# Kernel optimization log

Hardware: AMD Instinct MI355X
Metric: run time of the kernel (lower is better)

The kernel has to match this reference:

```python
import jax, jax.numpy as jnp
import numpy as np

BN_EPS = 1e-5
INTERP_EPS = 1e-8


def setup_inputs() -> dict:
    key = jax.random.key(0)
    ks = jax.random.split(key, 8)
    B, N, S, D1, D2 = 8, 8192, 2048, 128, 256
    C_in, C_mid, C_out = D1 + D2, 256, 256
    return {
        "xyz1": jax.random.normal(ks[0], (B, 3, N), dtype=jnp.float32),
        "xyz2": jax.random.normal(ks[1], (B, 3, S), dtype=jnp.float32),
        "points1": jax.random.normal(ks[2], (B, D1, N), dtype=jnp.float32),
        "points2": jax.random.normal(ks[3], (B, D2, S), dtype=jnp.float32),
        "W0": jax.random.normal(ks[4], (C_mid, C_in), dtype=jnp.float32) * (1.0 / np.sqrt(C_in)),
        "b0": jnp.zeros((C_mid,), dtype=jnp.float32),
        "gamma0": jnp.ones((C_mid,), dtype=jnp.float32),
        "beta0": jnp.zeros((C_mid,), dtype=jnp.float32),
        "W1": jax.random.normal(ks[5], (C_out, C_mid), dtype=jnp.float32) * (1.0 / np.sqrt(C_mid)),
        "b1": jnp.zeros((C_out,), dtype=jnp.float32),
    }


def reference(xyz1, xyz2, points1, points2, W0, b0, gamma0, beta0, W1, b1):
    B, _, N = xyz1.shape
    S = xyz2.shape[2]
    x1 = jnp.transpose(xyz1, (0, 2, 1))  # (B, N, 3)
    x2 = jnpp = jnp.transpose(xyz2, (0, 2, 1))  # (B, S, 3)
    # squared distances: (B, N, S)
    d = (jnp.sum(x1 ** 2, -1)[:, :, None]
         + jnp.sum(x2 ** 2, -1)[:, None, :]
         - 2.0 * jnp.einsum('bnc,bsc->bns', x1, x2))
    # 3 nearest neighbors (fused top-3 instead of full sort; same math)
    neg_d, idx = jax.lax.top_k(-d, 3)  # (B, N, 3)
    dists = -neg_d
    recip = 1.0 / (dists + INTERP_EPS)
    weight = recip / jnp.sum(recip, axis=2, keepdims=True)  # (B, N, 3)
    p2t = jnp.transpose(points2, (0, 2, 1))  # (B, S, D2)
    D2 = p2t.shape[-1]
    gathered = jnp.take_along_axis(p2t, idx.reshape(B, N * 3, 1), axis=1).reshape(B, N, 3, D2)
    interp = jnp.einsum('bnkc,bnk->bcn', gathered, weight)  # (B, D2, N)
    new_points = jnp.concatenate([interp, points1], axis=1)  # (B, D2+D1, N)
    # conv0 (1x1) + BatchNorm (train mode, batch stats) + ReLU
    h = jnp.einsum('oc,bcn->bon', W0, new_points) + b0[None, :, None]
    mean = jnp.mean(h, axis=(0, 2), keepdims=True)
    var = jnp.mean((h - mean) ** 2, axis=(0, 2), keepdims=True)  # biased, as torch BN
    h = gamma0[None, :, None] * (h - mean) * jax.lax.rsqrt(var + BN_EPS) + beta0[None, :, None]
    h = jax.nn.relu(h)
    # conv1 (1x1) + Identity (module pairs conv1 with nn.Identity) + ReLU
    h = jnp.einsum('oc,bcn->bon', W1, h) + b1[None, :, None]
    return jax.nn.relu(h)
```

## Files before the change

kernel.cpp:

```cpp
#include <hip/hip_runtime.h>
#include <stdint.h>

constexpr int B = 8, N = 8192, S = 2048, D1 = 128, D2 = 256;
constexpr int CIN = 384, CMID = 256, COUT = 256;

typedef __attribute__((ext_vector_type(8))) _Float16 half8;
typedef __attribute__((ext_vector_type(4))) _Float16 half4;
typedef __attribute__((ext_vector_type(4))) float f32x4;

union HU { uint32_t u; _Float16 h[2]; };


__global__ __launch_bounds__(256) void k_top3(const float* __restrict__ xyz1,
                                              const float* __restrict__ xyz2,
                                              uint32_t* __restrict__ pw3) {
  __shared__ float md[4][3][64];
  __shared__ int mi[4][3][64];
  const int tid = threadIdx.x;
  const int wv = tid >> 6, lane = tid & 63;
  const int b = blockIdx.y;
  const int n = blockIdx.x * 64 + lane;
  const float* x1 = xyz1 + (size_t)b * 3 * N;
  const float ax = x1[n], ay = x1[n + N], az = x1[n + 2 * N];
  const float* x2 = xyz2 + (size_t)b * 3 * S;

  float d0 = 1e30f, d1 = 1e30f, d2 = 1e30f;
  int i0 = 0, i1 = 0, i2 = 0;
  const int s0 = wv * (S / 4), s1 = s0 + (S / 4);
#pragma unroll 8
  for (int s = s0; s < s1; ++s) {
    float sx = x2[s], sy = x2[s + S], sz = x2[s + 2 * S];
    float dx = ax - sx, dy = ay - sy, dz = az - sz;
    float d = dx * dx + dy * dy + dz * dz;
    if (d < d2) {
      if (d < d1) {
        d2 = d1; i2 = i1;
        if (d < d0) { d1 = d0; i1 = i0; d0 = d; i0 = s; }
        else        { d1 = d;  i1 = s; }
      } else { d2 = d; i2 = s; }
    }
  }
  md[wv][0][lane] = d0; mi[wv][0][lane] = i0;
  md[wv][1][lane] = d1; mi[wv][1][lane] = i1;
  md[wv][2][lane] = d2; mi[wv][2][lane] = i2;
  __syncthreads();
  if (tid < 64) {
    float e0 = md[0][0][tid], e1 = md[0][1][tid], e2 = md[0][2][tid];
    int j0 = mi[0][0][tid], j1 = mi[0][1][tid], j2 = mi[0][2][tid];
#pragma unroll
    for (int w = 1; w < 4; ++w)
#pragma unroll
      for (int k = 0; k < 3; ++k) {
        float d = md[w][k][tid];
        int i = mi[w][k][tid];
        if (d < e2) {
          if (d < e1) {
            e2 = e1; j2 = j1;
            if (d < e0) { e1 = e0; j1 = j0; e0 = d; j0 = i; }
            else        { e1 = d;  j1 = i; }
          } else { e2 = d; j2 = i; }
        }
      }
    float r0 = 1.0f / (e0 + 1e-8f), r1 = 1.0f / (e1 + 1e-8f), r2 = 1.0f / (e2 + 1e-8f);
    float inv = 1.0f / (r0 + r1 + r2);
    auto pack = [](int i, float w) -> uint32_t {
      uint32_t q = (uint32_t)(w * 2097152.0f + 0.5f);
      if (q > 0x1FFFFFu) q = 0x1FFFFFu;
      return ((uint32_t)i << 21) | q;
    };
    size_t base = ((size_t)b * N + blockIdx.x * 64 + tid) * 3;
    pw3[base]     = pack(j0, r0 * inv);
    pw3[base + 1] = pack(j1, r1 * inv);
    pw3[base + 2] = pack(j2, r2 * inv);
  }
}

__global__ __launch_bounds__(256) void k_G(const float* __restrict__ points2,
                                           const float* __restrict__ W0,
                                           float* __restrict__ dout) {
  __shared__ half8 A_lds[4][256];
  __shared__ half8 B_lds[4][32];
  __shared__ float CT[32][258];
  const int tid = threadIdx.x;
  const int b = blockIdx.x >> 6;
  const int s0 = (blockIdx.x & 63) * 32;
  f32x4 acc[4][2] = {};
  const int wv = tid >> 6, lane = tid & 63;
  const int ln = lane & 15, quad = lane >> 4;
  const int bn = tid & 31, bkc = tid >> 5;
  const int ar = tid >> 3, ac4 = tid & 7;

  for (int kk = 0; kk < 256; kk += 32) {
    __syncthreads();
#pragma unroll
    for (int p = 0; p < 8; ++p) {
      int row = ar + 32 * p;
      const float4 v = *(const float4*)(W0 + (size_t)row * CIN + kk + ac4 * 4);
      half4 hv = {(_Float16)v.x, (_Float16)v.y, (_Float16)v.z, (_Float16)v.w};
      *(half4*)((_Float16*)&A_lds[ac4 >> 1][row] + (ac4 & 1) * 4) = hv;
    }
    {
      half4 hv;
#pragma unroll
      for (int j = 0; j < 4; ++j)
        hv[j] = (_Float16)points2[((size_t)(b * 256 + kk + bkc * 4 + j)) * S + s0 + bn];
      *(half4*)((_Float16*)&B_lds[bkc >> 1][bn] + (bkc & 1) * 4) = hv;
    }
    __syncthreads();
    half8 af[4], bf[2];
#pragma unroll
    for (int i = 0; i < 4; ++i) af[i] = A_lds[quad][wv * 64 + i * 16 + ln];
#pragma unroll
    for (int j = 0; j < 2; ++j) bf[j] = B_lds[quad][j * 16 + ln];
#pragma unroll
    for (int i = 0; i < 4; ++i)
#pragma unroll
      for (int j = 0; j < 2; ++j)
        acc[i][j] = __builtin_amdgcn_mfma_f32_16x16x32_f16(af[i], bf[j], acc[i][j], 0, 0, 0);
  }
  __syncthreads();
#pragma unroll
  for (int i = 0; i < 4; ++i)
#pragma unroll
    for (int reg = 0; reg < 4; ++reg) {
      int row = wv * 64 + i * 16 + quad * 4 + reg;
#pragma unroll
      for (int j = 0; j < 2; ++j) CT[j * 16 + ln][row] = acc[i][j][reg];
    }
  __syncthreads();
  const int sl = tid >> 3, g = tid & 7;
  float* g0 = dout + ((size_t)(b * 256 + 128)) * 8192 + (size_t)(s0 + sl) * 256 + g * 32;
#pragma unroll
  for (int q = 0; q < 8; ++q)
    *(float4*)(g0 + q * 4) = *(const float4*)&CT[sl][g * 32 + q * 4];
}

__global__ __launch_bounds__(256) void k_interp(const uint32_t* __restrict__ pw3,
                                                const float* __restrict__ dout_c,
                                                uint32_t* __restrict__ dout_u) {
  __shared__ int sidx[96];
  __shared__ float sw[96];
  const int tid = threadIdx.x;
  const int b = blockIdx.x >> 8;
  const int n0 = (blockIdx.x & 255) * 32;
  if (tid < 96) {
    uint32_t p = pw3[((size_t)b * N + n0) * 3 + tid];
    sidx[tid] = (int)(p >> 21);
    sw[tid] = (float)(p & 0x1FFFFFu) * (1.0f / 2097152.0f);
  }
  __syncthreads();
  const int colL = tid >> 3, p = tid & 7;
  const float* Gb = dout_c + ((size_t)(b * 256 + 128)) * 8192;
  float a[32];
#pragma unroll
  for (int q = 0; q < 32; ++q) a[q] = 0.f;
#pragma unroll
  for (int k = 0; k < 3; ++k) {
    int j = sidx[colL * 3 + k];
    float w = sw[colL * 3 + k];
    const float* g = Gb + (size_t)j * 256 + p * 32;
#pragma unroll
    for (int q = 0; q < 8; ++q) {
      float4 v = *(const float4*)(g + q * 4);
      a[q * 4 + 0] += w * v.x; a[q * 4 + 1] += w * v.y;
      a[q * 4 + 2] += w * v.z; a[q * 4 + 3] += w * v.w;
    }
  }
#pragma unroll
  for (int q = 0; q < 16; ++q) {
    int cp = p * 16 + q;
    HU u;
    u.h[0] = (_Float16)a[2 * q];
    u.h[1] = (_Float16)a[2 * q + 1];
    dout_u[((size_t)(b * 256 + cp)) * 8192 + n0 + colL] = u.u;
  }
}

__global__ __launch_bounds__(256) void k_h(uint32_t* __restrict__ h2,
                                           float* __restrict__ dpart,
                                           const float* __restrict__ points1,
                                           const float* __restrict__ W0,
                                           const float* __restrict__ b0) {
  __shared__ half8 A_lds[4][256];
  __shared__ half8 B_lds[4][64];
  __shared__ float red_s[256], red_q[256], sb0[256];
  const int tid = threadIdx.x;
  const int b = blockIdx.x >> 7;
  const int cb = blockIdx.x & 127;
  const int n0 = cb * 64;
  sb0[tid] = b0[tid];
  f32x4 acc[4][4] = {};
  const int wv = tid >> 6, lane = tid & 63;
  const int ln = lane & 15, quad = lane >> 4;
  const int bn = tid & 63, bkc = tid >> 6;
  const int ar = tid >> 3, ac4 = tid & 7;

  for (int kk = 0; kk < 128; kk += 32) {
    __syncthreads();
#pragma unroll
    for (int p = 0; p < 8; ++p) {
      int row = ar + 32 * p;
      const float4 v = *(const float4*)(W0 + (size_t)row * CIN + 256 + kk + ac4 * 4);
      half4 hv = {(_Float16)v.x, (_Float16)v.y, (_Float16)v.z, (_Float16)v.w};
      *(half4*)((_Float16*)&A_lds[ac4 >> 1][row] + (ac4 & 1) * 4) = hv;
    }
    {
      half8 hv;
#pragma unroll
      for (int j = 0; j < 8; ++j)
        hv[j] = (_Float16)points1[((size_t)(b * D1 + kk + bkc * 8 + j)) * N + n0 + bn];
      B_lds[bkc][bn] = hv;
    }
    __syncthreads();
    half8 af[4], bf[4];
#pragma unroll
    for (int i = 0; i < 4; ++i) af[i] = A_lds[quad][wv * 64 + i * 16 + ln];
#pragma unroll
    for (int j = 0; j < 4; ++j) bf[j] = B_lds[quad][j * 16 + ln];
#pragma unroll
    for (int i = 0; i < 4; ++i)
#pragma unroll
      for (int j = 0; j < 4; ++j)
        acc[i][j] = __builtin_amdgcn_mfma_f32_16x16x32_f16(af[i], bf[j], acc[i][j], 0, 0, 0);
  }
#pragma unroll
  for (int i = 0; i < 4; ++i) {
    const int rb = wv * 64 + i * 16 + quad * 4;
    const int cp0 = rb >> 1;
    float rs[4] = {0.f, 0.f, 0.f, 0.f}, rq[4] = {0.f, 0.f, 0.f, 0.f};
#pragma unroll
    for (int jj = 0; jj < 4; ++jj) {
      const int col = n0 + jj * 16 + ln;
      size_t a0 = ((size_t)(b * 256 + cp0)) * 8192 + col;
      HU ua, ub;
      ua.u = h2[a0];
      ub.u = h2[a0 + 8192];
      _Float16 e0 = (_Float16)(acc[i][jj][0] + (float)ua.h[0] + sb0[rb + 0]);
      _Float16 e1 = (_Float16)(acc[i][jj][1] + (float)ua.h[1] + sb0[rb + 1]);
      _Float16 e2 = (_Float16)(acc[i][jj][2] + (float)ub.h[0] + sb0[rb + 2]);
      _Float16 e3 = (_Float16)(acc[i][jj][3] + (float)ub.h[1] + sb0[rb + 3]);
      HU o0, o1;
      o0.h[0] = e0; o0.h[1] = e1; o1.h[0] = e2; o1.h[1] = e3;
      h2[a0] = o0.u;
      h2[a0 + 8192] = o1.u;
      float f0 = (float)e0, f1 = (float)e1, f2 = (float)e2, f3 = (float)e3;
      rs[0] += f0; rq[0] += f0 * f0;
      rs[1] += f1; rq[1] += f1 * f1;
      rs[2] += f2; rq[2] += f2 * f2;
      rs[3] += f3; rq[3] += f3 * f3;
    }
#pragma unroll
    for (int reg = 0; reg < 4; ++reg) {
      float s = rs[reg], q = rq[reg];
#pragma unroll
      for (int m = 1; m < 16; m <<= 1) {
        s += __shfl_xor(s, m);
        q += __shfl_xor(q, m);
      }
      if (ln == 0) { red_s[rb + reg] = s; red_q[rb + reg] = q; }
    }
  }
  __syncthreads();
  float* part = dpart + ((size_t)(b * 256 + 192)) * 8192 + (size_t)cb * 512;
  part[tid] = red_s[tid];
  part[256 + tid] = red_q[tid];
}

__global__ __launch_bounds__(256) void k_bn(const float* __restrict__ dpart,
                                            const float* __restrict__ gamma,
                                            const float* __restrict__ beta,
                                            float* __restrict__ bna,
                                            float* __restrict__ bnb) {
  const int c = blockIdx.x;
  const int tid = threadIdx.x;
  float s = 0.f, q = 0.f;
#pragma unroll
  for (int u = tid; u < 1024; u += 256) {
    int b = u >> 7, cb = u & 127;
    const float* part = dpart + ((size_t)(b * 256 + 192)) * 8192 + (size_t)cb * 512;
    s += part[c];
    q += part[256 + c];
  }
#pragma unroll
  for (int m = 1; m < 64; m <<= 1) {
    s += __shfl_xor(s, m);
    q += __shfl_xor(q, m);
  }
  __shared__ float ls[4], lq[4];
  if ((tid & 63) == 0) { ls[tid >> 6] = s; lq[tid >> 6] = q; }
  __syncthreads();
  if (tid == 0) {
    float st = ls[0] + ls[1] + ls[2] + ls[3];
    float qt = lq[0] + lq[1] + lq[2] + lq[3];
    const float invn = 1.0f / (float)(B * N);
    float mean = st * invn;
    float var = qt * invn - mean * mean;
    float a = gamma[c] * rsqrtf(var + 1e-5f);
    bna[c] = a;
    bnb[c] = beta[c] - mean * a;
  }
}

__global__ __launch_bounds__(256) void k_fused1(const uint32_t* h2,
                                                const float* __restrict__ W1,
                                                const float* __restrict__ b1,
                                                const float* __restrict__ bna,
                                                const float* __restrict__ bnb,
                                                float* out) {
  __shared__ uint32_t Hh[32 * 65 * 4];
  __shared__ float sa[256], sb[256], sb1[256];
  const int tid = threadIdx.x;
  const int b = blockIdx.x >> 7;
  const int n0 = (blockIdx.x & 127) * 64;
  sa[tid] = bna[tid]; sb[tid] = bnb[tid]; sb1[tid] = b1[tid];
  __syncthreads();
  {
    const int col = tid & 63, cpb = tid >> 6;
#pragma unroll
    for (int q = 0; q < 32; ++q) {
      int cp = cpb * 32 + q;
      HU u;
      u.u = h2[((size_t)(b * 256 + cp)) * 8192 + n0 + col];
      int k0 = 2 * cp;
      float v0 = sa[k0] * (float)u.h[0] + sb[k0];
      float v1 = sa[k0 + 1] * (float)u.h[1] + sb[k0 + 1];
      HU o;
      o.h[0] = (_Float16)(v0 > 0.f ? v0 : 0.f);
      o.h[1] = (_Float16)(v1 > 0.f ? v1 : 0.f);
      Hh[((cp >> 2) * 65 + col) * 4 + (cp & 3)] = o.u;
    }
  }
  __syncthreads();
  f32x4 acc[4][4] = {};
  const int wv = tid >> 6, lane = tid & 63;
  const int ln = lane & 15, quad = lane >> 4;
  for (int kk = 0; kk < 256; kk += 32) {
    half8 af[4], bf[4];
#pragma unroll
    for (int i = 0; i < 4; ++i) {
      int row = wv * 64 + i * 16 + ln;
      const float* wr = W1 + (size_t)row * CMID + kk + quad * 8;
      float4 w0 = *(const float4*)wr;
      float4 w1v = *(const float4*)(wr + 4);
      af[i] = half8{(_Float16)w0.x, (_Float16)w0.y, (_Float16)w0.z, (_Float16)w0.w,
                    (_Float16)w1v.x, (_Float16)w1v.y, (_Float16)w1v.z, (_Float16)w1v.w};
    }
#pragma unroll
    for (int j = 0; j < 4; ++j)
      bf[j] = *(const half8*)&Hh[(((kk >> 3) + quad) * 65 + j * 16 + ln) * 4];
#pragma unroll
    for (int i = 0; i < 4; ++i)
#pragma unroll
      for (int j = 0; j < 4; ++j)
        acc[i][j] = __builtin_amdgcn_mfma_f32_16x16x32_f16(af[i], bf[j], acc[i][j], 0, 0, 0);
  }
#pragma unroll
  for (int i = 0; i < 4; ++i) {
    const int rb = wv * 64 + i * 16 + quad * 4;
#pragma unroll
    for (int reg = 0; reg < 4; ++reg) {
      int row = rb + reg;
      float bias = sb1[row];
      float* orow = out + ((size_t)(b * 256 + row)) * 8192 + n0;
#pragma unroll
      for (int j = 0; j < 4; ++j)
        orow[j * 16 + ln] = fmaxf(acc[i][j][reg] + bias, 0.f);
    }
  }
}

extern "C" void kernel_launch(void* const* d_in, const int* in_sizes, int n_in,
                              void* d_out, int out_size, void* d_ws, size_t ws_size,
                              hipStream_t stream) {
  const float* xyz1 = (const float*)d_in[0];
  const float* xyz2 = (const float*)d_in[1];
  const float* points1 = (const float*)d_in[2];
  const float* points2 = (const float*)d_in[3];
  const float* W0 = (const float*)d_in[4];
  const float* b0 = (const float*)d_in[5];
  const float* gamma0 = (const float*)d_in[6];
  const float* beta0 = (const float*)d_in[7];
  const float* W1 = (const float*)d_in[8];
  const float* b1 = (const float*)d_in[9];
  float* out = (float*)d_out;

  char* ws = (char*)d_ws;
  float* bna = (float*)ws;
  float* bnb = (float*)(ws + 1024);
  uint32_t* pw3 = (uint32_t*)(ws + 2048);

  k_top3<<<dim3(N / 64, B), 256, 0, stream>>>(xyz1, xyz2, pw3);
  k_G<<<dim3(B * 64), 256, 0, stream>>>(points2, W0, out);
  k_interp<<<dim3(B * N / 32), 256, 0, stream>>>(pw3, out, (uint32_t*)out);
  k_h<<<dim3(B * N / 64), 256, 0, stream>>>((uint32_t*)out, out, points1, W0, b0);
  k_bn<<<dim3(256), 256, 0, stream>>>(out, gamma0, beta0, bna, bnb);
  k_fused1<<<dim3(B * N / 64), 256, 0, stream>>>((const uint32_t*)out, W1, b1,
                                                 bna, bnb, out);
}
```

Measured before the change: 375.3 us.

## Stage xyz2 with norms in LDS and use branchless expanded-distance top-3

The top-3 search kernel now loads each batch's query points into shared memory as float4 (x, y, z, |s|^2) once per block. The inner loop computes a partial distance with three FMAs using the expanded form, adding the query norm only at the end. The branchy insertion sort is replaced by branchless selects plus med3/min updates. This cuts global loads, ALU work and divergence in the hot loop, at the cost of 32KB of LDS per block, which may lower occupancy, and slight numerical differences in the distances.

```diff
diff --git a/kernel.cpp b/kernel.cpp
--- a/kernel.cpp
+++ b/kernel.cpp
@@ -14,8 +14,10 @@
 __global__ __launch_bounds__(256) void k_top3(const float* __restrict__ xyz1,
                                               const float* __restrict__ xyz2,
                                               uint32_t* __restrict__ pw3) {
+  __shared__ float4 Pq[S];
   __shared__ float md[4][3][64];
   __shared__ int mi[4][3][64];
+  __shared__ float snrm[64];
   const int tid = threadIdx.x;
   const int wv = tid >> 6, lane = tid & 63;
   const int b = blockIdx.y;
@@ -24,44 +26,57 @@
   const float ax = x1[n], ay = x1[n + N], az = x1[n + 2 * N];
   const float* x2 = xyz2 + (size_t)b * 3 * S;
 
-  float d0 = 1e30f, d1 = 1e30f, d2 = 1e30f;
-  int i0 = 0, i1 = 0, i2 = 0;
+  for (int j = tid; j < S; j += 256) {
+    float sx = x2[j], sy = x2[j + S], sz = x2[j + 2 * S];
+    Pq[j] = float4{sx, sy, sz, sx * sx + sy * sy + sz * sz};
+  }
+  if (wv == 0) snrm[lane] = ax * ax + ay * ay + az * az;
+  __syncthreads();
+
+  const float nax = -2.f * ax, nay = -2.f * ay, naz = -2.f * az;
+  float e0 = 1e30f, e1 = 1e30f, e2 = 1e30f;
+  int j0 = 0, j1 = 0, j2 = 0;
   const int s0 = wv * (S / 4), s1 = s0 + (S / 4);
 #pragma unroll 8
   for (int s = s0; s < s1; ++s) {
-    float sx = x2[s], sy = x2[s + S], sz = x2[s + 2 * S];
-    float dx = ax - sx, dy = ay - sy, dz = az - sz;
-    float d = dx * dx + dy * dy + dz * dz;
-    if (d < d2) {
-      if (d < d1) {
-        d2 = d1; i2 = i1;
-        if (d < d0) { d1 = d0; i1 = i0; d0 = d; i0 = s; }
-        else        { d1 = d;  i1 = s; }
-      } else { d2 = d; i2 = s; }
-    }
-  }
-  md[wv][0][lane] = d0; mi[wv][0][lane] = i0;
-  md[wv][1][lane] = d1; mi[wv][1][lane] = i1;
-  md[wv][2][lane] = d2; mi[wv][2][lane] = i2;
+    const float4 v = Pq[s];
+    const float d = fmaf(nax, v.x, fmaf(nay, v.y, fmaf(naz, v.z, v.w)));
+    const bool c0 = d < e0, c1 = d < e1, c2 = d < e2;
+    const int t2 = c1 ? j1 : s;
+    const int t1 = c0 ? j0 : s;
+    j2 = c2 ? t2 : j2;
+    j1 = c1 ? t1 : j1;
+    j0 = c0 ? s : j0;
+    e2 = __builtin_amdgcn_fmed3f(e1, e2, d);
+    e1 = __builtin_amdgcn_fmed3f(e0, e1, d);
+    e0 = fminf(e0, d);
+  }
+  md[wv][0][lane] = e0; mi[wv][0][lane] = j0;
+  md[wv][1][lane] = e1; mi[wv][1][lane] = j1;
+  md[wv][2][lane] = e2; mi[wv][2][lane] = j2;
   __syncthreads();
   if (tid < 64) {
-    float e0 = md[0][0][tid], e1 = md[0][1][tid], e2 = md[0][2][tid];
-    int j0 = mi[0][0][tid], j1 = mi[0][1][tid], j2 = mi[0][2][tid];
+    float f0 = md[0][0][tid], f1 = md[0][1][tid], f2 = md[0][2][tid];
+    int g0 = mi[0][0][tid], g1 = mi[0][1][tid], g2 = mi[0][2][tid];
 #pragma unroll
     for (int w = 1; w < 4; ++w)
 #pragma unroll
       for (int k = 0; k < 3; ++k) {
         float d = md[w][k][tid];
         int i = mi[w][k][tid];
-        if (d < e2) {
-          if (d < e1) {
-            e2 = e1; j2 = j1;
-            if (d < e0) { e1 = e0; j1 = j0; e0 = d; j0 = i; }
-            else        { e1 = d;  j1 = i; }
-          } else { e2 = d; j2 = i; }
+        if (d < f2) {
+          if (d < f1) {
+            f2 = f1; g2 = g1;
+            if (d < f0) { f1 = f0; g1 = g0; f0 = d; g0 = i; }
+            else        { f1 = d;  g1 = i; }
+          } else { f2 = d; g2 = i; }
         }
       }
-    float r0 = 1.0f / (e0 + 1e-8f), r1 = 1.0f / (e1 + 1e-8f), r2 = 1.0f / (e2 + 1e-8f);
+    const float rn = snrm[tid];
+    float q0 = fmaxf(f0 + rn, 0.f);
+    float q1 = fmaxf(f1 + rn, 0.f);
+    float q2 = fmaxf(f2 + rn, 0.f);
+    float r0 = 1.0f / (q0 + 1e-8f), r1 = 1.0f / (q1 + 1e-8f), r2 = 1.0f / (q2 + 1e-8f);
     float inv = 1.0f / (r0 + r1 + r2);
     auto pack = [](int i, float w) -> uint32_t {
       uint32_t q = (uint32_t)(w * 2097152.0f + 0.5f);
@@ -69,9 +84,9 @@
       return ((uint32_t)i << 21) | q;
     };
     size_t base = ((size_t)b * N + blockIdx.x * 64 + tid) * 3;
-    pw3[base]     = pack(j0, r0 * inv);
-    pw3[base + 1] = pack(j1, r1 * inv);
-    pw3[base + 2] = pack(j2, r2 * inv);
+    pw3[base]     = pack(g0, r0 * inv);
+    pw3[base + 1] = pack(g1, r1 * inv);
+    pw3[base + 2] = pack(g2, r2 * inv);
   }
 }
 
```

Result: faster. 341.5 us (-9.0%).
